# Performance work log

Hardware: AMD Instinct MI355X
Metric: run time of the kernel (lower is better)

## Reference

```python
import jax, jax.numpy as jnp
import numpy as np

DIM = 768
EPS = 1e-06


def _layernorm(x, gamma, beta):
    # LayerNorm over last axis (channels), eps=EPS, elementwise affine
    mu = jnp.mean(x, axis=-1, keepdims=True)
    var = jnp.mean(jnp.square(x - mu), axis=-1, keepdims=True)
    return (x - mu) * jax.lax.rsqrt(var + EPS) * gamma + beta


def setup_inputs() -> dict:
    key = jax.random.key(0)
    ks = jax.random.split(key, 10)
    B, C, H, W = 16, DIM, 32, 32
    s = 1.0 / np.sqrt(C)  # mimic Conv2d default init scale
    return {
        "x": jax.random.normal(ks[0], (B, C, H, W), dtype=jnp.float32),
        "W1": jax.random.uniform(ks[1], (C, C), jnp.float32, -s, s),
        "b1": jax.random.uniform(ks[2], (C,), jnp.float32, -s, s),
        "g1": jnp.ones((C,), jnp.float32),
        "beta1": jnp.zeros((C,), jnp.float32),
        "W2": jax.random.uniform(ks[3], (C, C), jnp.float32, -s, s),
        "b2": jax.random.uniform(ks[4], (C,), jnp.float32, -s, s),
        "g2": jnp.ones((C,), jnp.float32),
        "beta2": jnp.zeros((C,), jnp.float32),
        "W3": jax.random.uniform(ks[5], (C, C), jnp.float32, -s, s),
        "b3": jax.random.uniform(ks[6], (C,), jnp.float32, -s, s),
    }


def reference(x, W1, b1, g1, beta1, W2, b2, g2, beta2, W3, b3):
    # x: [B, C, H, W] (NCHW). Work in NHWC; 1x1 conv == channel matmul.
    h = jnp.transpose(x, (0, 2, 3, 1))  # [B, H, W, C]
    h = jnp.einsum("bhwc,oc->bhwo", h, W1) + b1
    h = jax.nn.gelu(_layernorm(h, g1, beta1), approximate=False)
    h = jnp.einsum("bhwc,oc->bhwo", h, W2) + b2
    h = jax.nn.gelu(_layernorm(h, g2, beta2), approximate=False)
    h = jnp.einsum("bhwc,oc->bhwo", h, W3) + b3
    return jnp.transpose(h, (0, 3, 1, 2))  # back to NCHW
```

## Files before the change

kernel.cpp:

```cpp
#include <hip/hip_runtime.h>
#include <hip/hip_bf16.h>

typedef __bf16 bf16;
typedef __bf16 bf16x4 __attribute__((ext_vector_type(4)));
typedef __bf16 bf16x8 __attribute__((ext_vector_type(8)));
typedef float f32x4 __attribute__((ext_vector_type(4)));

#define DIM 768
#define HW 1024
#define BATCH 16
#define M_TOTAL (BATCH * HW)
#define NT 24

__global__ void wcvt3_kernel(const float4* __restrict__ w1, const float4* __restrict__ w2,
                             const float4* __restrict__ w3,
                             bf16x4* __restrict__ o1, bf16x4* __restrict__ o2,
                             bf16x4* __restrict__ o3) {
    const int b = blockIdx.x;
    const int which = b / 576;
    const int i = (b % 576) * 256 + threadIdx.x;
    const float4* w = which == 0 ? w1 : which == 1 ? w2 : w3;
    bf16x4* o = which == 0 ? o1 : which == 1 ? o2 : o3;
    float4 v = w[i];
    bf16x4 r = { (bf16)v.x, (bf16)v.y, (bf16)v.z, (bf16)v.w };
    o[i] = r;
}

__global__ void transpose_cvt_kernel(const float* __restrict__ x, bf16* __restrict__ xb) {
    __shared__ float tile[32][33];
    const int b = blockIdx.z;
    const int hw0 = blockIdx.x * 32;
    const int c0 = blockIdx.y * 32;
    const int tx = threadIdx.x, ty = threadIdx.y;

    const float* src = x + ((size_t)b * DIM + c0) * HW + hw0;
#pragma unroll
    for (int j = 0; j < 4; j++)
        tile[ty + 8 * j][tx] = src[(size_t)(ty + 8 * j) * HW + tx];
    __syncthreads();
    bf16* dst = xb + ((size_t)b * HW + hw0) * DIM + c0;
#pragma unroll
    for (int j = 0; j < 4; j++)
        dst[(size_t)(ty + 8 * j) * DIM + tx] = (bf16)tile[tx][ty + 8 * j];
}

template <int MODE>
__global__ __launch_bounds__(256) void gemm_kernel(
    const bf16* __restrict__ A,
    const bf16* __restrict__ Bw,
    const float* __restrict__ bias,
    void* __restrict__ out)
{
    constexpr int K = DIM;
    __shared__ bf16 As[3][128][32];
    __shared__ bf16 Bs[3][128][32];

    const int t = threadIdx.x;
    const int lane = t & 63;
    const int wave = t >> 6;
    const int wr = wave >> 1, wc = wave & 1;
    const int m0 = blockIdx.x * 128;
    const int n0 = blockIdx.y * 128;

    f32x4 acc[4][4] = {};

    const int srow = t >> 2;
    const int glin = t & 3;
    const int fr = lane & 15;
    const int kb = (lane >> 4) * 4;

    const int s_rd = (fr >> 1) & 3;
    const int g0 = kb >> 3;
    const int rem = kb & 7;
    const int offLo = ((g0 ^ s_rd) << 3) + rem;
    const int offHi = (((g0 + 2) ^ s_rd) << 3) + rem;

    auto stage = [&](int kt, int buf) {
        const int k0 = kt * 32;
#pragma unroll
        for (int i = 0; i < 2; i++) {
            const int r = srow + i * 64;
            const int gsrc = glin ^ ((r >> 1) & 3);
            __builtin_amdgcn_global_load_lds(
                (const __attribute__((address_space(1))) void*)(A + (size_t)(m0 + r) * K + k0 + gsrc * 8),
                (__attribute__((address_space(3))) void*)&As[buf][r][glin * 8], 16, 0, 0);
            __builtin_amdgcn_global_load_lds(
                (const __attribute__((address_space(1))) void*)(Bw + (size_t)(n0 + r) * K + k0 + gsrc * 8),
                (__attribute__((address_space(3))) void*)&Bs[buf][r][glin * 8], 16, 0, 0);
        }
    };

    stage(0, 0);
    stage(1, 1);

    int c0 = 0, c1 = 1, c2 = 2;
    for (int kt = 0; kt < NT; ++kt) {
        if (kt < NT - 2) {
            stage(kt + 2, c2);
            asm volatile("s_waitcnt vmcnt(8)" ::: "memory");
        } else if (kt == NT - 2) {
            asm volatile("s_waitcnt vmcnt(4)" ::: "memory");
        } else {
            asm volatile("s_waitcnt vmcnt(0)" ::: "memory");
        }
        __builtin_amdgcn_s_barrier();
        __builtin_amdgcn_sched_barrier(0);

        bf16x8 aF[4], bF[4];
#pragma unroll
        for (int mi = 0; mi < 4; mi++) {
            const bf16* p = &As[c0][wr * 64 + mi * 16 + fr][0];
            bf16x4 lo = *(const bf16x4*)(p + offLo);
            bf16x4 hi = *(const bf16x4*)(p + offHi);
            aF[mi] = __builtin_shufflevector(lo, hi, 0, 1, 2, 3, 4, 5, 6, 7);
        }
#pragma unroll
        for (int ni = 0; ni < 4; ni++) {
            const bf16* p = &Bs[c0][wc * 64 + ni * 16 + fr][0];
            bf16x4 lo = *(const bf16x4*)(p + offLo);
            bf16x4 hi = *(const bf16x4*)(p + offHi);
            bF[ni] = __builtin_shufflevector(lo, hi, 0, 1, 2, 3, 4, 5, 6, 7);
        }
        __builtin_amdgcn_s_setprio(1);
#pragma unroll
        for (int mi = 0; mi < 4; mi++)
#pragma unroll
            for (int ni = 0; ni < 4; ni++)
                acc[mi][ni] = __builtin_amdgcn_mfma_f32_16x16x32_bf16(aF[mi], bF[ni], acc[mi][ni], 0, 0, 0);
        __builtin_amdgcn_s_setprio(0);
        __builtin_amdgcn_sched_barrier(0);
        __builtin_amdgcn_s_barrier();

        const int tmp = c0; c0 = c1; c1 = c2; c2 = tmp;
    }

    const int fq = lane >> 4;
    if (MODE == 0) {
        bf16* o = (bf16*)out;
#pragma unroll
        for (int mi = 0; mi < 4; mi++) {
            const int row = m0 + wr * 64 + mi * 16 + fq * 4;
#pragma unroll
            for (int ni = 0; ni < 4; ni++) {
                const int col = n0 + wc * 64 + ni * 16 + fr;
                const float bv = bias[col];
#pragma unroll
                for (int r = 0; r < 4; r++)
                    o[(size_t)(row + r) * DIM + col] = (bf16)(acc[mi][ni][r] + bv);
            }
        }
    } else {
        float* o = (float*)out;
#pragma unroll
        for (int mi = 0; mi < 4; mi++) {
            const int n_base = m0 + wr * 64 + mi * 16 + fq * 4;
            const int b = n_base >> 10;
            const int hw = n_base & 1023;
#pragma unroll
            for (int ni = 0; ni < 4; ni++) {
                const int col = n0 + wc * 64 + ni * 16 + fr;
                const float bv = bias[col];
                f32x4 v = acc[mi][ni] + bv;
                *(f32x4*)(o + ((size_t)b * DIM + col) * HW + hw) = v;
            }
        }
    }
}

__global__ __launch_bounds__(256) void ln_gelu_kernel(
    bf16* __restrict__ h, const float* __restrict__ g, const float* __restrict__ beta)
{
    const int wave = threadIdx.x >> 6;
    const int lane = threadIdx.x & 63;
    const int n = blockIdx.x * 4 + wave;
    bf16* row = h + (size_t)n * DIM;

    float v[12];
    float s = 0.f, ss = 0.f;
#pragma unroll
    for (int j = 0; j < 3; j++) {
        bf16x4 x = *(const bf16x4*)(row + j * 256 + lane * 4);
#pragma unroll
        for (int i = 0; i < 4; i++) {
            float f = (float)x[i];
            v[j * 4 + i] = f;
            s += f;
            ss += f * f;
        }
    }
#pragma unroll
    for (int off = 32; off > 0; off >>= 1) {
        s += __shfl_xor(s, off);
        ss += __shfl_xor(ss, off);
    }
    const float mu = s * (1.f / DIM);
    const float var = ss * (1.f / DIM) - mu * mu;
    const float rstd = rsqrtf(var + 1e-6f);

#pragma unroll
    for (int j = 0; j < 3; j++) {
        bf16x4 r;
#pragma unroll
        for (int i = 0; i < 4; i++) {
            const int c = j * 256 + lane * 4 + i;
            float y = (v[j * 4 + i] - mu) * rstd * g[c] + beta[c];
            y = 0.5f * y * (1.f + erff(y * 0.70710678118f));
            r[i] = (bf16)y;
        }
        *(bf16x4*)(row + j * 256 + lane * 4) = r;
    }
}

extern "C" void kernel_launch(void* const* d_in, const int* in_sizes, int n_in,
                              void* d_out, int out_size, void* d_ws, size_t ws_size,
                              hipStream_t stream) {
    const float* x   = (const float*)d_in[0];
    const float* W1  = (const float*)d_in[1];
    const float* b1  = (const float*)d_in[2];
    const float* g1  = (const float*)d_in[3];
    const float* be1 = (const float*)d_in[4];
    const float* W2  = (const float*)d_in[5];
    const float* b2  = (const float*)d_in[6];
    const float* g2  = (const float*)d_in[7];
    const float* be2 = (const float*)d_in[8];
    const float* W3  = (const float*)d_in[9];
    const float* b3  = (const float*)d_in[10];
    float* out = (float*)d_out;

    bf16* Wb1  = (bf16*)d_ws;
    bf16* Wb2  = Wb1 + (size_t)DIM * DIM;
    bf16* Wb3  = Wb2 + (size_t)DIM * DIM;
    bf16* buf0 = Wb3 + (size_t)DIM * DIM;
    bf16* buf1 = buf0 + (size_t)M_TOTAL * DIM;

    wcvt3_kernel<<<1728, 256, 0, stream>>>((const float4*)W1, (const float4*)W2, (const float4*)W3,
                                           (bf16x4*)Wb1, (bf16x4*)Wb2, (bf16x4*)Wb3);

    transpose_cvt_kernel<<<dim3(32, 24, 16), dim3(32, 8), 0, stream>>>(x, buf0);

    dim3 ggrid(M_TOTAL / 128, DIM / 128);
    gemm_kernel<0><<<ggrid, 256, 0, stream>>>(buf0, Wb1, b1, buf1);
    ln_gelu_kernel<<<M_TOTAL / 4, 256, 0, stream>>>(buf1, g1, be1);
    gemm_kernel<0><<<ggrid, 256, 0, stream>>>(buf1, Wb2, b2, buf0);
    ln_gelu_kernel<<<M_TOTAL / 4, 256, 0, stream>>>(buf0, g2, be2);
    gemm_kernel<1><<<ggrid, 256, 0, stream>>>(buf0, Wb3, b3, out);
}
```

Before: 171.1 us.

## Permute K layout so GEMM fragments load as single 16-byte LDS reads

Activations and weights are stored with a permuted channel order within each 32-wide K chunk, so each lane's MFMA fragment is contiguous and is read with one bf16x8 LDS load instead of two bf16x4 loads plus a shuffle. The permutation is applied consistently in the weight conversion, the input transpose, the GEMM epilogue and the LayerNorm gamma/beta indexing. The GEMM also gets a 1D grid remapped so concurrent blocks are grouped by XCD, a new swizzle, one barrier per K step instead of two, and launch bounds targeting 3 blocks per CU. The cost is more index arithmetic in the epilogue and LN kernel, and correctness rests on every stage agreeing on the permutation.

New measurement: 163.7 us. -4.3%, faster.

```diff
diff --git a/kernel.cpp b/kernel.cpp
--- a/kernel.cpp
+++ b/kernel.cpp
@@ -10,20 +10,28 @@
 #define HW 1024
 #define BATCH 16
 #define M_TOTAL (BATCH * HW)
-#define NT 24
+#define NKT 24
+
+#define AS1 __attribute__((address_space(1)))
+#define AS3 __attribute__((address_space(3)))
+
 
 __global__ void wcvt3_kernel(const float4* __restrict__ w1, const float4* __restrict__ w2,
                              const float4* __restrict__ w3,
-                             bf16x4* __restrict__ o1, bf16x4* __restrict__ o2,
-                             bf16x4* __restrict__ o3) {
+                             bf16x8* __restrict__ o1, bf16x8* __restrict__ o2,
+                             bf16x8* __restrict__ o3) {
     const int b = blockIdx.x;
-    const int which = b / 576;
-    const int i = (b % 576) * 256 + threadIdx.x;
+    const int which = b / 288;
+    const int i = (b % 288) * 256 + threadIdx.x;
     const float4* w = which == 0 ? w1 : which == 1 ? w2 : w3;
-    bf16x4* o = which == 0 ? o1 : which == 1 ? o2 : o3;
-    float4 v = w[i];
-    bf16x4 r = { (bf16)v.x, (bf16)v.y, (bf16)v.z, (bf16)v.w };
-    o[i] = r;
+    bf16x8* o = which == 0 ? o1 : which == 1 ? o2 : o3;
+    const int row = i / 96, br = i % 96;
+    const int q = br >> 2, g = br & 3;
+    float4 lo = w[row * 192 + q * 8 + g];
+    float4 hi = w[row * 192 + q * 8 + g + 4];
+    bf16x8 r = { (bf16)lo.x, (bf16)lo.y, (bf16)lo.z, (bf16)lo.w,
+                 (bf16)hi.x, (bf16)hi.y, (bf16)hi.z, (bf16)hi.w };
+    o[row * 96 + br] = r;
 }
 
 __global__ void transpose_cvt_kernel(const float* __restrict__ x, bf16* __restrict__ xb) {
@@ -38,14 +46,15 @@
     for (int j = 0; j < 4; j++)
         tile[ty + 8 * j][tx] = src[(size_t)(ty + 8 * j) * HW + tx];
     __syncthreads();
+    const int ptx = (((tx & 15) >> 2) << 3) + (tx & 3) + ((tx >> 4) << 2);
     bf16* dst = xb + ((size_t)b * HW + hw0) * DIM + c0;
 #pragma unroll
     for (int j = 0; j < 4; j++)
-        dst[(size_t)(ty + 8 * j) * DIM + tx] = (bf16)tile[tx][ty + 8 * j];
+        dst[(size_t)(ty + 8 * j) * DIM + ptx] = (bf16)tile[tx][ty + 8 * j];
 }
 
 template <int MODE>
-__global__ __launch_bounds__(256) void gemm_kernel(
+__global__ __launch_bounds__(256, 3) void gemm_kernel(
     const bf16* __restrict__ A,
     const bf16* __restrict__ Bw,
     const float* __restrict__ bias,
@@ -59,67 +68,56 @@
     const int lane = t & 63;
     const int wave = t >> 6;
     const int wr = wave >> 1, wc = wave & 1;
-    const int m0 = blockIdx.x * 128;
-    const int n0 = blockIdx.y * 128;
+
+    const int bid = blockIdx.x;
+    const int virt = (bid & 7) * 96 + (bid >> 3);
+    const int mI = virt / 6;
+    const int m0 = mI * 128;
+    const int n0 = (virt - mI * 6) * 128;
+
+    const int fr = lane & 15;
+    const int fq = lane >> 4;
 
     f32x4 acc[4][4] = {};
 
-    const int srow = t >> 2;
-    const int glin = t & 3;
-    const int fr = lane & 15;
-    const int kb = (lane >> 4) * 4;
-
-    const int s_rd = (fr >> 1) & 3;
-    const int g0 = kb >> 3;
-    const int rem = kb & 7;
-    const int offLo = ((g0 ^ s_rd) << 3) + rem;
-    const int offHi = (((g0 + 2) ^ s_rd) << 3) + rem;
+    const int sr = t >> 2;
+    const int sb = t & 3;
 
     auto stage = [&](int kt, int buf) {
         const int k0 = kt * 32;
 #pragma unroll
-        for (int i = 0; i < 2; i++) {
-            const int r = srow + i * 64;
-            const int gsrc = glin ^ ((r >> 1) & 3);
+        for (int j = 0; j < 2; j++) {
+            const int r = sr + j * 64;
+            const int gs = sb ^ ((r ^ (r >> 2)) & 3);
             __builtin_amdgcn_global_load_lds(
-                (const __attribute__((address_space(1))) void*)(A + (size_t)(m0 + r) * K + k0 + gsrc * 8),
-                (__attribute__((address_space(3))) void*)&As[buf][r][glin * 8], 16, 0, 0);
+                (const AS1 void*)(A + (size_t)(m0 + r) * K + k0 + gs * 8),
+                (AS3 void*)&As[buf][r][sb * 8], 16, 0, 0);
             __builtin_amdgcn_global_load_lds(
-                (const __attribute__((address_space(1))) void*)(Bw + (size_t)(n0 + r) * K + k0 + gsrc * 8),
-                (__attribute__((address_space(3))) void*)&Bs[buf][r][glin * 8], 16, 0, 0);
+                (const AS1 void*)(Bw + (size_t)(n0 + r) * K + k0 + gs * 8),
+                (AS3 void*)&Bs[buf][r][sb * 8], 16, 0, 0);
         }
     };
 
     stage(0, 0);
     stage(1, 1);
+    asm volatile("s_waitcnt vmcnt(4)" ::: "memory");
+    __builtin_amdgcn_s_barrier();
+    __builtin_amdgcn_sched_barrier(0);
 
     int c0 = 0, c1 = 1, c2 = 2;
-    for (int kt = 0; kt < NT; ++kt) {
-        if (kt < NT - 2) {
-            stage(kt + 2, c2);
-            asm volatile("s_waitcnt vmcnt(8)" ::: "memory");
-        } else if (kt == NT - 2) {
-            asm volatile("s_waitcnt vmcnt(4)" ::: "memory");
-        } else {
-            asm volatile("s_waitcnt vmcnt(0)" ::: "memory");
-        }
-        __builtin_amdgcn_s_barrier();
-        __builtin_amdgcn_sched_barrier(0);
+    for (int kt = 0; kt < NKT; ++kt) {
+        if (kt + 2 < NKT) stage(kt + 2, c2);
 
         bf16x8 aF[4], bF[4];
 #pragma unroll
         for (int mi = 0; mi < 4; mi++) {
-            const bf16* p = &As[c0][wr * 64 + mi * 16 + fr][0];
-            bf16x4 lo = *(const bf16x4*)(p + offLo);
-            bf16x4 hi = *(const bf16x4*)(p + offHi);
-            aF[mi] = __builtin_shufflevector(lo, hi, 0, 1, 2, 3, 4, 5, 6, 7);
+            const int R = wr * 64 + mi * 16 + fr;
+            aF[mi] = *(const bf16x8*)(&As[c0][R][0] + ((fq ^ ((R ^ (R >> 2)) & 3)) << 3));
         }
 #pragma unroll
         for (int ni = 0; ni < 4; ni++) {
-            const bf16* p = &Bs[c0][wc * 64 + ni * 16 + fr][0];
-            bf16x4 lo = *(const bf16x4*)(p + offLo);
-            bf16x4 hi = *(const bf16x4*)(p + offHi);
-            bF[ni] = __builtin_shufflevector(lo, hi, 0, 1, 2, 3, 4, 5, 6, 7);
+            const int R = wc * 64 + ni * 16 + fr;
+            bF[ni] = *(const bf16x8*)(&Bs[c0][R][0] + ((fq ^ ((R ^ (R >> 2)) & 3)) << 3));
         }
         __builtin_amdgcn_s_setprio(1);
 #pragma unroll
@@ -128,13 +126,16 @@
             for (int ni = 0; ni < 4; ni++)
                 acc[mi][ni] = __builtin_amdgcn_mfma_f32_16x16x32_bf16(aF[mi], bF[ni], acc[mi][ni], 0, 0, 0);
         __builtin_amdgcn_s_setprio(0);
-        __builtin_amdgcn_sched_barrier(0);
-        __builtin_amdgcn_s_barrier();
-
+
+        if (kt < NKT - 1) {
+            if (kt + 2 < NKT) { asm volatile("s_waitcnt vmcnt(4)" ::: "memory"); }
+            else              { asm volatile("s_waitcnt vmcnt(0)" ::: "memory"); }
+            __builtin_amdgcn_s_barrier();
+            __builtin_amdgcn_sched_barrier(0);
+        }
         const int tmp = c0; c0 = c1; c1 = c2; c2 = tmp;
     }
 
-    const int fq = lane >> 4;
     if (MODE == 0) {
         bf16* o = (bf16*)out;
 #pragma unroll
@@ -143,25 +144,25 @@
 #pragma unroll
             for (int ni = 0; ni < 4; ni++) {
                 const int col = n0 + wc * 64 + ni * 16 + fr;
+                const int pcol = n0 + wc * 64 + ((ni >> 1) << 5) + ((fr >> 2) << 3)
+                               + (fr & 3) + ((ni & 1) << 2);
                 const float bv = bias[col];
 #pragma unroll
                 for (int r = 0; r < 4; r++)
-                    o[(size_t)(row + r) * DIM + col] = (bf16)(acc[mi][ni][r] + bv);
+                    o[(size_t)(row + r) * DIM + pcol] = (bf16)(acc[mi][ni][r] + bv);
             }
         }
     } else {
         float* o = (float*)out;
 #pragma unroll
         for (int mi = 0; mi < 4; mi++) {
-            const int n_base = m0 + wr * 64 + mi * 16 + fq * 4;
-            const int b = n_base >> 10;
-            const int hw = n_base & 1023;
+            const int nb = m0 + wr * 64 + mi * 16 + (lane >> 4) * 4;
+            const int bI = nb >> 10, hw = nb & 1023;
 #pragma unroll
             for (int ni = 0; ni < 4; ni++) {
                 const int col = n0 + wc * 64 + ni * 16 + fr;
-                const float bv = bias[col];
-                f32x4 v = acc[mi][ni] + bv;
-                *(f32x4*)(o + ((size_t)b * DIM + col) * HW + hw) = v;
+                f32x4 v = acc[mi][ni] + bias[col];
+                *(f32x4*)(o + ((size_t)bI * DIM + col) * HW + hw) = v;
             }
         }
     }
@@ -203,7 +204,10 @@
 #pragma unroll
         for (int i = 0; i < 4; i++) {
             const int c = j * 256 + lane * 4 + i;
-            float y = (v[j * 4 + i] - mu) * rstd * g[c] + beta[c];
+            const int p = (lane * 4 + i) & 31;
+            const int kk = ((p >> 3) << 2) + (p & 7) + ((p & 4) ? 12 : 0);
+            const int gi = (c & ~31) + kk;
+            float y = (v[j * 4 + i] - mu) * rstd * g[gi] + beta[gi];
             y = 0.5f * y * (1.f + erff(y * 0.70710678118f));
             r[i] = (bf16)y;
         }
@@ -233,12 +237,12 @@
     bf16* buf0 = Wb3 + (size_t)DIM * DIM;
     bf16* buf1 = buf0 + (size_t)M_TOTAL * DIM;
 
-    wcvt3_kernel<<<1728, 256, 0, stream>>>((const float4*)W1, (const float4*)W2, (const float4*)W3,
-                                           (bf16x4*)Wb1, (bf16x4*)Wb2, (bf16x4*)Wb3);
+    wcvt3_kernel<<<864, 256, 0, stream>>>((const float4*)W1, (const float4*)W2, (const float4*)W3,
+                                          (bf16x8*)Wb1, (bf16x8*)Wb2, (bf16x8*)Wb3);
 
     transpose_cvt_kernel<<<dim3(32, 24, 16), dim3(32, 8), 0, stream>>>(x, buf0);
 
-    dim3 ggrid(M_TOTAL / 128, DIM / 128);
+    const int ggrid = (M_TOTAL / 128) * (DIM / 128);
     gemm_kernel<0><<<ggrid, 256, 0, stream>>>(buf0, Wb1, b1, buf1);
     ln_gelu_kernel<<<M_TOTAL / 4, 256, 0, stream>>>(buf1, g1, be1);
     gemm_kernel<0><<<ggrid, 256, 0, stream>>>(buf1, Wb2, b2, buf0);
```
